# Performance work log

Measured on AMD Instinct MI355X. Metric: run time of the kernel, lower is better.

## Reference

```python
import jax, jax.numpy as jnp
import numpy as np

N_NODES = 50000
N_EDGES = 800000
N_GRAPHS = 512
D = 128


def _gcn_layer(x, W, b, src, dst, norm):
    # PyG GCNConv: h = x @ W; out[i] = sum_{j->i} norm_ji * h[j]; out += b
    h = x @ W                                   # [N, D]
    msg = h[src] * norm[:, None]                # [E+N, D] gathered messages
    out = jax.ops.segment_sum(msg, dst, num_segments=N_NODES)
    return out + b


def setup_inputs() -> dict:
    key = jax.random.key(0)
    ks = jax.random.split(key, 9)
    inp = {
        "x": jax.random.normal(ks[0], (N_NODES, D), dtype=jnp.float32),
        "W1": jax.random.normal(ks[1], (D, D), dtype=jnp.float32) * 0.05,
        "b1": jax.random.normal(ks[2], (D,), dtype=jnp.float32) * 0.05,
        "W2": jax.random.normal(ks[3], (D, D), dtype=jnp.float32) * 0.05,
        "b2": jax.random.normal(ks[4], (D,), dtype=jnp.float32) * 0.05,
        "W3": jax.random.normal(ks[5], (D, D), dtype=jnp.float32) * 0.05,
        "b3": jax.random.normal(ks[6], (D,), dtype=jnp.float32) * 0.05,
        "edge_index": jax.random.randint(ks[7], (2, N_EDGES), 0, N_NODES, dtype=jnp.int64),
        "batch_vec": jnp.sort(jax.random.randint(ks[8], (N_NODES,), 0, N_GRAPHS, dtype=jnp.int64)),
    }
    return inp


def reference(x, W1, b1, W2, b2, W3, b3, edge_index, batch_vec):
    # Add self-loops (GCNConv default) and compute symmetric normalization.
    loops = jnp.arange(N_NODES, dtype=edge_index.dtype)
    src = jnp.concatenate([edge_index[0], loops])   # [E+N]
    dst = jnp.concatenate([edge_index[1], loops])   # [E+N]
    deg = jax.ops.segment_sum(jnp.ones_like(dst, dtype=x.dtype), dst,
                              num_segments=N_NODES)
    dis = jnp.where(deg > 0, jax.lax.rsqrt(jnp.maximum(deg, 1.0)), 0.0)
    norm = dis[src] * dis[dst]                      # [E+N]

    h = jax.nn.relu(_gcn_layer(x, W1, b1, src, dst, norm))
    h = jax.nn.relu(_gcn_layer(h, W2, b2, src, dst, norm))
    h = jax.nn.relu(_gcn_layer(h, W3, b3, src, dst, norm))

    # global_add_pool: per-graph sum over nodes.
    return jax.ops.segment_sum(h, batch_vec, num_segments=N_GRAPHS)  # [G, D]
```

## Files before the change

kernel.cpp:

```cpp
#include <hip/hip_runtime.h>

#define N_NODES 50000
#define N_EDGES 800000
#define N_GRAPHS 512
#define DIM 128
#define N_PAD 50048

#define BW_LOG 9
#define BWID 512
#define NB ((N_NODES + BWID - 1) / BWID)
#define CHUNK 4096
#define NCHUNK ((N_EDGES + CHUNK - 1) / CHUNK)

typedef unsigned int uint;
typedef unsigned short ushort;
typedef __attribute__((ext_vector_type(8))) short bf16x8;
typedef __attribute__((ext_vector_type(4))) float f32x4;

__device__ __forceinline__ ushort f2bf(float f) {
    uint u = __float_as_uint(f);
    return (ushort)((u + 0x7fffu + ((u >> 16) & 1u)) >> 16);
}
__device__ __forceinline__ float bf2f(ushort h) { return __uint_as_float((uint)h << 16); }
__device__ __forceinline__ float bflo(uint p) { return __uint_as_float(p << 16); }
__device__ __forceinline__ float bfhi(uint p) { return __uint_as_float(p & 0xffff0000u); }


__global__ __launch_bounds__(256) void bhist_k(const int* __restrict__ dst,
                                               int* __restrict__ bcnt_pad, int e) {
    __shared__ int h[NB];
    int t = threadIdx.x;
    for (int i = t; i < NB; i += 256) h[i] = 0;
    __syncthreads();
    int base = blockIdx.x * CHUNK;
    for (int i = t; i < CHUNK; i += 256) {
        int idx = base + i;
        if (idx < e) atomicAdd(&h[dst[idx] >> BW_LOG], 1);
    }
    __syncthreads();
    for (int i = t; i < NB; i += 256)
        if (h[i]) atomicAdd(&bcnt_pad[i << 4], h[i]);
}

__global__ void bscan_k(const int* __restrict__ bcnt_pad, int* __restrict__ bbase,
                        int* __restrict__ bcur_pad) {
    __shared__ int v[128];
    int t = threadIdx.x;
    int x = (t < NB) ? bcnt_pad[t << 4] : 0;
    v[t] = x;
    __syncthreads();
    for (int o = 1; o < 128; o <<= 1) {
        int val = v[t];
        int add = (t >= o) ? v[t - o] : 0;
        __syncthreads();
        v[t] = val + add;
        __syncthreads();
    }
    if (t < NB) {
        int excl = (t == 0) ? 0 : v[t - 1];
        bbase[t] = excl;
        bcur_pad[t << 4] = excl;
    }
    if (t == NB - 1) bbase[NB] = v[t];
}

__global__ __launch_bounds__(256) void bscat_k(const int* __restrict__ src,
                                               const int* __restrict__ dst,
                                               int* __restrict__ bcur_pad,
                                               uint* __restrict__ stage, int e) {
    __shared__ int h[NB];
    __shared__ int bb[NB];
    __shared__ int lc[NB];
    int t = threadIdx.x;
    for (int i = t; i < NB; i += 256) h[i] = 0;
    __syncthreads();
    int base = blockIdx.x * CHUNK;
    for (int i = t; i < CHUNK; i += 256) {
        int idx = base + i;
        if (idx < e) atomicAdd(&h[dst[idx] >> BW_LOG], 1);
    }
    __syncthreads();
    for (int i = t; i < NB; i += 256) {
        int c = h[i];
        bb[i] = c ? atomicAdd(&bcur_pad[i << 4], c) : 0;
        lc[i] = 0;
    }
    __syncthreads();
    for (int i = t; i < CHUNK; i += 256) {
        int idx = base + i;
        if (idx < e) {
            int d = dst[idx];
            int b = d >> BW_LOG;
            int r = atomicAdd(&lc[b], 1);
            stage[bb[b] + r] = ((uint)src[idx] << BW_LOG) | (uint)(d & (BWID - 1));
        }
    }
}

__global__ __launch_bounds__(256) void csr_k(const uint* __restrict__ stage,
                                             const int* __restrict__ bbase,
                                             int* __restrict__ row_ptr,
                                             float* __restrict__ dis,
                                             int* __restrict__ col) {
    __shared__ int hist[BWID];
    __shared__ int excl[BWID];
    __shared__ int ws[256];
    int b = blockIdx.x, t = threadIdx.x;
    int beg = bbase[b], end = bbase[b + 1];
    for (int i = t; i < BWID; i += 256) hist[i] = 0;
    __syncthreads();
    for (int i = beg + t; i < end; i += 256)
        atomicAdd(&hist[stage[i] & (BWID - 1)], 1);
    __syncthreads();
    int s = hist[2 * t] + hist[2 * t + 1];
    ws[t] = s;
    __syncthreads();
    for (int o = 1; o < 256; o <<= 1) {
        int v = ws[t];
        int add = (t >= o) ? ws[t - o] : 0;
        __syncthreads();
        ws[t] = v + add;
        __syncthreads();
    }
    int pre = (t == 0) ? 0 : ws[t - 1];
    excl[2 * t] = pre;
    excl[2 * t + 1] = pre + hist[2 * t];
    __syncthreads();
    int node0 = b * BWID;
    for (int i = t; i < BWID; i += 256) {
        int node = node0 + i;
        if (node < N_NODES) {
            row_ptr[node] = beg + excl[i];
            dis[node] = rsqrtf((float)(hist[i] + 1));
        } else if (node == N_NODES) {
            row_ptr[node] = beg + excl[i];
        }
    }
    __syncthreads();
    for (int i = t; i < BWID; i += 256) hist[i] = excl[i];
    __syncthreads();
    for (int i = beg + t; i < end; i += 256) {
        uint p = stage[i];
        int d9 = p & (BWID - 1);
        int r = atomicAdd(&hist[d9], 1);
        col[beg + r] = (int)(p >> BW_LOG);
    }
}


__global__ void wconv_k(const float* __restrict__ Wa, const float* __restrict__ Wb,
                        const float* __restrict__ Wc, ushort* __restrict__ Whi,
                        ushort* __restrict__ Wlo) {
    int i = blockIdx.x * 256 + threadIdx.x;
    int layer = i >> 14, r = i & 16383;
    const float* W = layer == 0 ? Wa : (layer == 1 ? Wb : Wc);
    int k = r >> 7, nn = r & 127;
    float w = W[r];
    ushort h = f2bf(w);
    size_t o = (size_t)layer * DIM * DIM + nn * 128 + k;
    Whi[o] = h;
    Wlo[o] = f2bf(w - bf2f(h));
}


template <typename TIn>
__global__ __launch_bounds__(256) void gemm_mfma_k(const TIn* __restrict__ X,
                                                   const ushort* __restrict__ Whi,
                                                   const ushort* __restrict__ Wlo,
                                                   const float* __restrict__ dis,
                                                   ushort* __restrict__ H, int n) {
    __shared__ __align__(16) ushort lds[128 * 136];
    int t = threadIdx.x;

    auto stageW = [&](const ushort* Wsw) {
#pragma unroll
        for (int j = 0; j < 8; j++) {
            int idx8 = t + j * 256;
            int nn = idx8 >> 4;
            int k0 = (idx8 & 15) * 8;
            uint4 v = ((const uint4*)Wsw)[idx8];
            *(uint4*)&lds[nn * 136 + k0] = v;
        }
    };

    stageW(Whi);

    int w = t >> 6, l = t & 63;
    int quad = l >> 4, lr = l & 15;
    int arow = blockIdx.x * 64 + w * 16 + lr;
    int srow = arow < n ? arow : n - 1;

    bf16x8 a[4], alo[4];
#pragma unroll
    for (int q = 0; q < 4; q++) {
        if constexpr (sizeof(TIn) == 4) {
            const float4* xp = (const float4*)(X + (size_t)srow * DIM + q * 32 + quad * 8);
            float4 v0 = xp[0], v1 = xp[1];
            float f[8] = {v0.x, v0.y, v0.z, v0.w, v1.x, v1.y, v1.z, v1.w};
            bf16x8 ah, al;
#pragma unroll
            for (int j = 0; j < 8; j++) {
                ushort h = f2bf(f[j]);
                ah[j] = (short)h;
                al[j] = (short)f2bf(f[j] - bf2f(h));
            }
            a[q] = ah;
            alo[q] = al;
        } else {
            a[q] = *(const bf16x8*)(X + (size_t)srow * DIM + q * 32 + quad * 8);
        }
    }

    f32x4 acc[8];
#pragma unroll
    for (int c = 0; c < 8; c++) acc[c] = (f32x4){0.f, 0.f, 0.f, 0.f};

    __syncthreads();
#pragma unroll
    for (int q = 0; q < 4; q++) {
#pragma unroll
        for (int c = 0; c < 8; c++) {
            bf16x8 b = *(const bf16x8*)&lds[(c * 16 + lr) * 136 + q * 32 + quad * 8];
            acc[c] = __builtin_amdgcn_mfma_f32_16x16x32_bf16(a[q], b, acc[c], 0, 0, 0);
            if constexpr (sizeof(TIn) == 4)
                acc[c] = __builtin_amdgcn_mfma_f32_16x16x32_bf16(alo[q], b, acc[c], 0, 0, 0);
        }
    }

    __syncthreads();
    stageW(Wlo);
    __syncthreads();
#pragma unroll
    for (int q = 0; q < 4; q++) {
#pragma unroll
        for (int c = 0; c < 8; c++) {
            bf16x8 b = *(const bf16x8*)&lds[(c * 16 + lr) * 136 + q * 32 + quad * 8];
            acc[c] = __builtin_amdgcn_mfma_f32_16x16x32_bf16(a[q], b, acc[c], 0, 0, 0);
        }
    }

    float dsc[4];
    int orow0 = blockIdx.x * 64 + w * 16 + quad * 4;
#pragma unroll
    for (int r = 0; r < 4; r++) {
        int rr = orow0 + r;
        if (rr > n - 1) rr = n - 1;
        dsc[r] = dis[rr];
    }

    __syncthreads();
#pragma unroll
    for (int c = 0; c < 8; c++) {
#pragma unroll
        for (int r = 0; r < 4; r++) {
            int rl = w * 16 + quad * 4 + r;
            lds[rl * 136 + c * 16 + lr] = f2bf(acc[c][r] * dsc[r]);
        }
    }
    __syncthreads();
#pragma unroll
    for (int j = 0; j < 4; j++) {
        int idx = t + j * 256;
        int rl = idx >> 4, sl = idx & 15;
        int grow = blockIdx.x * 64 + rl;
        if (grow < n) {
            uint4 v = *(const uint4*)&lds[rl * 136 + sl * 8];
            ((uint4*)(H + (size_t)grow * DIM))[sl] = v;
        }
    }
}


#define COLCAP 1024

#define AGG_STAGE                                                                \
    int first_n = blockIdx.x * 16;                                               \
    int cbase = row_ptr[first_n];                                                \
    int last_n = first_n + 16;                                                   \
    if (last_n > n) last_n = n;                                                  \
    int ccnt = row_ptr[last_n] - cbase;                                          \
    if (ccnt > COLCAP) ccnt = COLCAP;                                            \
    for (int i = threadIdx.x; i < ccnt; i += 256) cols_s[i] = col[cbase + i];    \
    __syncthreads();

#define AGG_EDGE8(E0, PRED)                                                      \
    {                                                                            \
        int c_[8];                                                               \
        float w_[8];                                                             \
        uint4 p_[8];                                                             \
        _Pragma("unroll") for (int j = 0; j < 8; j++) {                          \
            int idx = E0 + j;                                                    \
            w_[j] = 1.f;                                                         \
            if (PRED) {                                                          \
                w_[j] = (idx < end) ? 1.f : 0.f;                                 \
                idx = idx < end ? idx : end - 1;                                 \
            }                                                                    \
            int li = idx - cbase;                                                \
            c_[j] = (li < COLCAP) ? cols_s[li] : col[idx];                       \
        }                                                                        \
        _Pragma("unroll") for (int j = 0; j < 8; j++) {                          \
            p_[j] = *(const uint4*)(Hl + (size_t)c_[j] * DIM);                   \
        }                                                                        \
        _Pragma("unroll") for (int j = 0; j < 8; j++) {                          \
            a0 += w_[j] * bflo(p_[j].x);                                         \
            a1 += w_[j] * bfhi(p_[j].x);                                         \
            a2 += w_[j] * bflo(p_[j].y);                                         \
            a3 += w_[j] * bfhi(p_[j].y);                                         \
            a4 += w_[j] * bflo(p_[j].z);                                         \
            a5 += w_[j] * bfhi(p_[j].z);                                         \
            a6 += w_[j] * bflo(p_[j].w);                                         \
            a7 += w_[j] * bfhi(p_[j].w);                                         \
        }                                                                        \
    }

#define AGG_BODY                                                                 \
    const ushort* Hl = H + lane * 8;                                             \
    float dn = dis[node];                                                        \
    int beg = row_ptr[node], end = row_ptr[node + 1];                            \
    uint4 pw = *(const uint4*)(Hl + (size_t)node * DIM);                         \
    a0 = bflo(pw.x); a1 = bfhi(pw.x);                                            \
    a2 = bflo(pw.y); a3 = bfhi(pw.y);                                            \
    a4 = bflo(pw.z); a5 = bfhi(pw.z);                                            \
    a6 = bflo(pw.w); a7 = bfhi(pw.w);                                            \
    int e = beg;                                                                 \
    for (; e + 7 < end; e += 8) AGG_EDGE8(e, 0)                                  \
    if (e < end) AGG_EDGE8(e, 1)                                                 \
    a0 = fmaxf(a0 * dn + bias[d0], 0.f);                                         \
    a1 = fmaxf(a1 * dn + bias[d0 + 1], 0.f);                                     \
    a2 = fmaxf(a2 * dn + bias[d0 + 2], 0.f);                                     \
    a3 = fmaxf(a3 * dn + bias[d0 + 3], 0.f);                                     \
    a4 = fmaxf(a4 * dn + bias[d0 + 4], 0.f);                                     \
    a5 = fmaxf(a5 * dn + bias[d0 + 5], 0.f);                                     \
    a6 = fmaxf(a6 * dn + bias[d0 + 6], 0.f);                                     \
    a7 = fmaxf(a7 * dn + bias[d0 + 7], 0.f);

__global__ __launch_bounds__(256) void agg_k(const ushort* __restrict__ H,
                                             const int* __restrict__ row_ptr,
                                             const int* __restrict__ col,
                                             const float* __restrict__ dis,
                                             const float* __restrict__ bias,
                                             ushort* __restrict__ Out, int n) {
    __shared__ int cols_s[COLCAP];
    int node = blockIdx.x * 16 + (threadIdx.x >> 4);
    int lane = threadIdx.x & 15;
    AGG_STAGE
    if (node >= n) return;
    int d0 = lane * 8;
    float a0, a1, a2, a3, a4, a5, a6, a7;
    AGG_BODY
    uint4 o;
    o.x = (uint)f2bf(a0) | ((uint)f2bf(a1) << 16);
    o.y = (uint)f2bf(a2) | ((uint)f2bf(a3) << 16);
    o.z = (uint)f2bf(a4) | ((uint)f2bf(a5) << 16);
    o.w = (uint)f2bf(a6) | ((uint)f2bf(a7) << 16);
    *(uint4*)(Out + (size_t)node * DIM + d0) = o;
}

__global__ __launch_bounds__(256) void agg_pool_k(const ushort* __restrict__ H,
                                                  const int* __restrict__ row_ptr,
                                                  const int* __restrict__ col,
                                                  const float* __restrict__ dis,
                                                  const float* __restrict__ bias,
                                                  const int* __restrict__ batch,
                                                  float* __restrict__ Out, int n) {
    __shared__ float acc[DIM];
    __shared__ int cols_s[COLCAP];
    int t = threadIdx.x;
    int node = blockIdx.x * 16 + (t >> 4);
    int lane = t & 15;
    int d0 = lane * 8;
    float a0 = 0.f, a1 = 0.f, a2 = 0.f, a3 = 0.f, a4 = 0.f, a5 = 0.f, a6 = 0.f, a7 = 0.f;
    AGG_STAGE
    int g = -1;
    if (node < n) {
        AGG_BODY
        g = batch[node];
    }
    int first = blockIdx.x * 16;
    int last = first + 15 < n ? first + 15 : n - 1;
    int g0 = batch[first], g1 = batch[last];
    for (int gr = g0; gr <= g1; gr++) {
        if (t < DIM) acc[t] = 0.f;
        __syncthreads();
        if (g == gr) {
            atomicAdd(&acc[d0], a0);
            atomicAdd(&acc[d0 + 1], a1);
            atomicAdd(&acc[d0 + 2], a2);
            atomicAdd(&acc[d0 + 3], a3);
            atomicAdd(&acc[d0 + 4], a4);
            atomicAdd(&acc[d0 + 5], a5);
            atomicAdd(&acc[d0 + 6], a6);
            atomicAdd(&acc[d0 + 7], a7);
        }
        __syncthreads();
        if (t < DIM) atomicAdd(&Out[gr * DIM + t], acc[t]);
        __syncthreads();
    }
}


extern "C" void kernel_launch(void* const* d_in, const int* in_sizes, int n_in,
                              void* d_out, int out_size, void* d_ws, size_t ws_size,
                              hipStream_t stream) {
    const float* x  = (const float*)d_in[0];
    const float* W1 = (const float*)d_in[1];
    const float* b1 = (const float*)d_in[2];
    const float* W2 = (const float*)d_in[3];
    const float* b2 = (const float*)d_in[4];
    const float* W3 = (const float*)d_in[5];
    const float* b3 = (const float*)d_in[6];
    const int*   ei = (const int*)d_in[7];
    const int*   bv = (const int*)d_in[8];
    float* out = (float*)d_out;

    const int N = N_NODES, E = N_EDGES;

    char* p = (char*)d_ws;
    auto alloc = [&](size_t bytes) -> void* {
        void* r = (void*)p;
        p += (bytes + 255) & ~(size_t)255;
        return r;
    };
    int*    bcnt_pad = (int*)alloc((size_t)NB * 16 * 4);
    int*    bcur_pad = (int*)alloc((size_t)NB * 16 * 4);
    int*    bbase    = (int*)alloc((size_t)(NB + 1) * 4);
    int*    row_ptr  = (int*)alloc((size_t)(N + 1) * 4);
    float*  dis      = (float*)alloc((size_t)N * 4);
    uint*   stage    = (uint*)alloc((size_t)E * 4);
    int*    col      = (int*)alloc((size_t)E * 4);
    ushort* B1       = (ushort*)alloc((size_t)N_PAD * DIM * 2);
    ushort* B2       = (ushort*)alloc((size_t)N_PAD * DIM * 2);

    ushort* Whi = (ushort*)stage;
    ushort* Wlo = Whi + (size_t)3 * DIM * DIM;

    const int* src = ei;
    const int* dst = ei + E;

    hipMemsetAsync(d_out, 0, (size_t)N_GRAPHS * DIM * sizeof(float), stream);
    hipMemsetAsync(bcnt_pad, 0, (size_t)NB * 16 * 4, stream);

    bhist_k<<<NCHUNK, 256, 0, stream>>>(dst, bcnt_pad, E);
    bscan_k<<<1, 128, 0, stream>>>(bcnt_pad, bbase, bcur_pad);
    bscat_k<<<NCHUNK, 256, 0, stream>>>(src, dst, bcur_pad, stage, E);
    csr_k<<<NB, 256, 0, stream>>>(stage, bbase, row_ptr, dis, col);

    wconv_k<<<192, 256, 0, stream>>>(W1, W2, W3, Whi, Wlo);

    int gemm_grid = N_PAD / 64;
    int agg_grid  = (N + 15) / 16;

    gemm_mfma_k<float><<<gemm_grid, 256, 0, stream>>>(x, Whi, Wlo, dis, B1, N);
    agg_k<<<agg_grid, 256, 0, stream>>>(B1, row_ptr, col, dis, b1, B2, N);

    gemm_mfma_k<ushort><<<gemm_grid, 256, 0, stream>>>(B2, Whi + (size_t)DIM * DIM,
                                                       Wlo + (size_t)DIM * DIM, dis, B1, N);
    agg_k<<<agg_grid, 256, 0, stream>>>(B1, row_ptr, col, dis, b2, B2, N);

    gemm_mfma_k<ushort><<<gemm_grid, 256, 0, stream>>>(B2, Whi + (size_t)2 * DIM * DIM,
                                                       Wlo + (size_t)2 * DIM * DIM, dis, B1, N);
    agg_pool_k<<<agg_grid, 256, 0, stream>>>(B1, row_ptr, col, dis, b3, bv, out, N);
}
```

Before: 289.5 us.

## Split hidden features into four column slabs for cache-friendly aggregation

The intermediate node features are stored as four separate 32-column slabs (N_PAD x 32 each) instead of row-major 128 columns. The aggregation kernels get a second grid dimension that handles one slab per block, with 4 threads per node instead of 16. Each gathered slab is a quarter of the full feature array, so random neighbour gathers are more likely to hit in L2/MALL. The shared-memory staging of column indices is removed, and the edge list and row pointers are now read four times, once per slab.

```diff
diff --git a/kernel.cpp b/kernel.cpp
--- a/kernel.cpp
+++ b/kernel.cpp
@@ -11,6 +11,8 @@
 #define NB ((N_NODES + BWID - 1) / BWID)
 #define CHUNK 4096
 #define NCHUNK ((N_EDGES + CHUNK - 1) / CHUNK)
+
+#define QOFF(q) ((size_t)(q) * N_PAD * 32)
 
 typedef unsigned int uint;
 typedef unsigned short ushort;
@@ -207,7 +209,7 @@
             a[q] = ah;
             alo[q] = al;
         } else {
-            a[q] = *(const bf16x8*)(X + (size_t)srow * DIM + q * 32 + quad * 8);
+            a[q] = *(const bf16x8*)(X + QOFF(q) + (size_t)srow * 32 + quad * 8);
         }
     }
 
@@ -265,23 +267,11 @@
         int grow = blockIdx.x * 64 + rl;
         if (grow < n) {
             uint4 v = *(const uint4*)&lds[rl * 136 + sl * 8];
-            ((uint4*)(H + (size_t)grow * DIM))[sl] = v;
-        }
-    }
-}
-
-
-#define COLCAP 1024
-
-#define AGG_STAGE                                                                \
-    int first_n = blockIdx.x * 16;                                               \
-    int cbase = row_ptr[first_n];                                                \
-    int last_n = first_n + 16;                                                   \
-    if (last_n > n) last_n = n;                                                  \
-    int ccnt = row_ptr[last_n] - cbase;                                          \
-    if (ccnt > COLCAP) ccnt = COLCAP;                                            \
-    for (int i = threadIdx.x; i < ccnt; i += 256) cols_s[i] = col[cbase + i];    \
-    __syncthreads();
+            *(uint4*)(H + QOFF(sl >> 2) + (size_t)grow * 32 + (sl & 3) * 8) = v;
+        }
+    }
+}
+
 
 #define AGG_EDGE8(E0, PRED)                                                      \
     {                                                                            \
@@ -295,11 +285,10 @@
                 w_[j] = (idx < end) ? 1.f : 0.f;                                 \
                 idx = idx < end ? idx : end - 1;                                 \
             }                                                                    \
-            int li = idx - cbase;                                                \
-            c_[j] = (li < COLCAP) ? cols_s[li] : col[idx];                       \
+            c_[j] = col[idx];                                                    \
         }                                                                        \
         _Pragma("unroll") for (int j = 0; j < 8; j++) {                          \
-            p_[j] = *(const uint4*)(Hl + (size_t)c_[j] * DIM);                   \
+            p_[j] = *(const uint4*)(Hl + (size_t)c_[j] * 32);                    \
         }                                                                        \
         _Pragma("unroll") for (int j = 0; j < 8; j++) {                          \
             a0 += w_[j] * bflo(p_[j].x);                                         \
@@ -314,10 +303,10 @@
     }
 
 #define AGG_BODY                                                                 \
-    const ushort* Hl = H + lane * 8;                                             \
+    const ushort* Hl = H + QOFF(q) + d0l;                                        \
     float dn = dis[node];                                                        \
     int beg = row_ptr[node], end = row_ptr[node + 1];                            \
-    uint4 pw = *(const uint4*)(Hl + (size_t)node * DIM);                         \
+    uint4 pw = *(const uint4*)(Hl + (size_t)node * 32);                          \
     a0 = bflo(pw.x); a1 = bfhi(pw.x);                                            \
     a2 = bflo(pw.y); a3 = bfhi(pw.y);                                            \
     a4 = bflo(pw.z); a5 = bfhi(pw.z);                                            \
@@ -325,14 +314,14 @@
     int e = beg;                                                                 \
     for (; e + 7 < end; e += 8) AGG_EDGE8(e, 0)                                  \
     if (e < end) AGG_EDGE8(e, 1)                                                 \
-    a0 = fmaxf(a0 * dn + bias[d0], 0.f);                                         \
-    a1 = fmaxf(a1 * dn + bias[d0 + 1], 0.f);                                     \
-    a2 = fmaxf(a2 * dn + bias[d0 + 2], 0.f);                                     \
-    a3 = fmaxf(a3 * dn + bias[d0 + 3], 0.f);                                     \
-    a4 = fmaxf(a4 * dn + bias[d0 + 4], 0.f);                                     \
-    a5 = fmaxf(a5 * dn + bias[d0 + 5], 0.f);                                     \
-    a6 = fmaxf(a6 * dn + bias[d0 + 6], 0.f);                                     \
-    a7 = fmaxf(a7 * dn + bias[d0 + 7], 0.f);
+    a0 = fmaxf(a0 * dn + bias[q * 32 + d0l + 0], 0.f);                           \
+    a1 = fmaxf(a1 * dn + bias[q * 32 + d0l + 1], 0.f);                           \
+    a2 = fmaxf(a2 * dn + bias[q * 32 + d0l + 2], 0.f);                           \
+    a3 = fmaxf(a3 * dn + bias[q * 32 + d0l + 3], 0.f);                           \
+    a4 = fmaxf(a4 * dn + bias[q * 32 + d0l + 4], 0.f);                           \
+    a5 = fmaxf(a5 * dn + bias[q * 32 + d0l + 5], 0.f);                           \
+    a6 = fmaxf(a6 * dn + bias[q * 32 + d0l + 6], 0.f);                           \
+    a7 = fmaxf(a7 * dn + bias[q * 32 + d0l + 7], 0.f);
 
 __global__ __launch_bounds__(256) void agg_k(const ushort* __restrict__ H,
                                              const int* __restrict__ row_ptr,
@@ -340,12 +329,12 @@
                                              const float* __restrict__ dis,
                                              const float* __restrict__ bias,
                                              ushort* __restrict__ Out, int n) {
-    __shared__ int cols_s[COLCAP];
-    int node = blockIdx.x * 16 + (threadIdx.x >> 4);
-    int lane = threadIdx.x & 15;
-    AGG_STAGE
+    int q = blockIdx.y;
+    int t = threadIdx.x;
+    int node = blockIdx.x * 64 + (t >> 2);
+    int lane = t & 3;
     if (node >= n) return;
-    int d0 = lane * 8;
+    int d0l = lane * 8;
     float a0, a1, a2, a3, a4, a5, a6, a7;
     AGG_BODY
     uint4 o;
@@ -353,7 +342,7 @@
     o.y = (uint)f2bf(a2) | ((uint)f2bf(a3) << 16);
     o.z = (uint)f2bf(a4) | ((uint)f2bf(a5) << 16);
     o.w = (uint)f2bf(a6) | ((uint)f2bf(a7) << 16);
-    *(uint4*)(Out + (size_t)node * DIM + d0) = o;
+    *(uint4*)(Out + QOFF(q) + (size_t)node * 32 + d0l) = o;
 }
 
 __global__ __launch_bounds__(256) void agg_pool_k(const ushort* __restrict__ H,
@@ -363,37 +352,36 @@
                                                   const float* __restrict__ bias,
                                                   const int* __restrict__ batch,
                                                   float* __restrict__ Out, int n) {
-    __shared__ float acc[DIM];
-    __shared__ int cols_s[COLCAP];
-    int t = threadIdx.x;
-    int node = blockIdx.x * 16 + (t >> 4);
-    int lane = t & 15;
-    int d0 = lane * 8;
+    __shared__ float acc[32];
+    int q = blockIdx.y;
+    int t = threadIdx.x;
+    int node = blockIdx.x * 64 + (t >> 2);
+    int lane = t & 3;
+    int d0l = lane * 8;
     float a0 = 0.f, a1 = 0.f, a2 = 0.f, a3 = 0.f, a4 = 0.f, a5 = 0.f, a6 = 0.f, a7 = 0.f;
-    AGG_STAGE
     int g = -1;
     if (node < n) {
         AGG_BODY
         g = batch[node];
     }
-    int first = blockIdx.x * 16;
-    int last = first + 15 < n ? first + 15 : n - 1;
+    int first = blockIdx.x * 64;
+    int last = first + 63 < n ? first + 63 : n - 1;
     int g0 = batch[first], g1 = batch[last];
     for (int gr = g0; gr <= g1; gr++) {
-        if (t < DIM) acc[t] = 0.f;
+        if (t < 32) acc[t] = 0.f;
         __syncthreads();
         if (g == gr) {
-            atomicAdd(&acc[d0], a0);
-            atomicAdd(&acc[d0 + 1], a1);
-            atomicAdd(&acc[d0 + 2], a2);
-            atomicAdd(&acc[d0 + 3], a3);
-            atomicAdd(&acc[d0 + 4], a4);
-            atomicAdd(&acc[d0 + 5], a5);
-            atomicAdd(&acc[d0 + 6], a6);
-            atomicAdd(&acc[d0 + 7], a7);
-        }
-        __syncthreads();
-        if (t < DIM) atomicAdd(&Out[gr * DIM + t], acc[t]);
+            atomicAdd(&acc[d0l], a0);
+            atomicAdd(&acc[d0l + 1], a1);
+            atomicAdd(&acc[d0l + 2], a2);
+            atomicAdd(&acc[d0l + 3], a3);
+            atomicAdd(&acc[d0l + 4], a4);
+            atomicAdd(&acc[d0l + 5], a5);
+            atomicAdd(&acc[d0l + 6], a6);
+            atomicAdd(&acc[d0l + 7], a7);
+        }
+        __syncthreads();
+        if (t < 32) atomicAdd(&Out[gr * DIM + q * 32 + t], acc[t]);
         __syncthreads();
     }
 }
@@ -448,7 +436,7 @@
     wconv_k<<<192, 256, 0, stream>>>(W1, W2, W3, Whi, Wlo);
 
     int gemm_grid = N_PAD / 64;
-    int agg_grid  = (N + 15) / 16;
+    dim3 agg_grid((N + 63) / 64, 4);
 
     gemm_mfma_k<float><<<gemm_grid, 256, 0, stream>>>(x, Whi, Wlo, dis, B1, N);
     agg_k<<<agg_grid, 256, 0, stream>>>(B1, row_ptr, col, dis, b1, B2, N);
```

Result: no change. 285.7 us (-1.3%).
